# Kernel tuning notes

Hardware: AMD Instinct MI355X
Metric: run time of the kernel (lower is better)

The kernel has to match this reference:

```python
import jax, jax.numpy as jnp
import numpy as np

E = 65536      # num edges
T = 262144     # num triplets
H = 128        # hidden_channels
D = 64         # int_emb_size
C = 8          # basis_emb_size
NR = 6         # num_radial
NS = 7         # num_spherical
NB = 6         # len(bt_list) = num_BT + 1
BT_LIST = (-1, 0, 1, 2, 3, 4)
NBS = 1        # num_before_skip (also used for after-skip list in original code)


def setup_inputs() -> dict:
    key = jax.random.key(0)
    ks = iter(jax.random.split(key, 40))
    s = 0.05
    p = lambda shape: jax.random.normal(next(ks), shape, dtype=jnp.float32) * s
    inp = dict(
        x=jax.random.normal(next(ks), (E, H), dtype=jnp.float32),
        rbf=jax.random.normal(next(ks), (E, NR), dtype=jnp.float32),
        sbf=jax.random.normal(next(ks), (T, NS * NR), dtype=jnp.float32),
        idx_kj=jax.random.randint(next(ks), (T,), 0, E),
        idx_ji=jax.random.randint(next(ks), (T,), 0, E),
        bt=jax.random.randint(next(ks), (E,), 0, 5),
        lambda_d=1,
        alpha=jnp.float32(0.7),
        # per-branch stacked weights (6 branches)
        W_kj=p((NB, H, H)), b_kj=jnp.zeros((NB, H), jnp.float32),
        W_rbf1=p((NB, NR, C)), W_rbf2=p((NB, C, H)),
        W_sbf1=p((NB, NS * NR, C)), W_sbf2=p((NB, C, D)),
        W_down=p((NB, H, D)),
        W_ji=p((H, H)), b_ji=jnp.zeros((H,), jnp.float32),
        W_up=p((D, H)),
        rb1_w=p((NBS, H, H)), rb1_b=jnp.zeros((NBS, H), jnp.float32),
        rb2_w=p((NBS, H, H)), rb2_b=jnp.zeros((NBS, H), jnp.float32),
        W_lin=p((H, H)), b_lin=jnp.zeros((H,), jnp.float32),
        ra1_w=p((NBS, H, H)), ra1_b=jnp.zeros((NBS, H), jnp.float32),
        ra2_w=p((NBS, H, H)), ra2_b=jnp.zeros((NBS, H), jnp.float32),
    )
    return inp


def reference(x, rbf, sbf, idx_kj, idx_ji, bt, lambda_d, alpha,
              W_kj, b_kj, W_rbf1, W_rbf2, W_sbf1, W_sbf2, W_down,
              W_ji, b_ji, W_up, rb1_w, rb1_b, rb2_w, rb2_b,
              W_lin, b_lin, ra1_w, ra1_b, ra2_w, ra2_b):
    act = jax.nn.silu

    x_ji = act(x @ W_ji + b_ji)                                  # [E,H]

    # per-branch edge transforms, vectorized over the 6 branches (axis b)
    tmp = act(jnp.einsum('eh,bhg->beg', x, W_kj) + b_kj[:, None, :])   # [B,E,H]
    rbf_p = jnp.einsum('er,brc->bec', rbf, W_rbf1)                     # [B,E,C]
    rbf_p = jnp.einsum('bec,bcg->beg', rbf_p, W_rbf2)                  # [B,E,H]
    tmp = tmp * rbf_p
    down = act(jnp.einsum('beh,bhd->bed', tmp, W_down))                # [B,E,D]

    sbf_p = jnp.einsum('ts,bsc->btc', sbf, W_sbf1)                     # [B,T,C]
    sbf_p = jnp.einsum('btc,bcd->btd', sbf_p, W_sbf2)                  # [B,T,D]

    spe = down[:, idx_kj, :] * sbf_p                                   # [B,T,D]

    # last branch scattered with weight alpha
    x_kj_tot = alpha * jax.ops.segment_sum(spe[-1], idx_ji, num_segments=E)

    # per band-type masked scatter with weight (1 - alpha)
    bt_trip = bt[idx_kj]                                               # [T]
    for b, btv in enumerate(BT_LIST):
        m = (bt_trip == btv).astype(x.dtype)[:, None]
        x_kj_tot = x_kj_tot + (1.0 - alpha) * jax.ops.segment_sum(
            spe[b] * m, idx_ji, num_segments=E)

    x_kj = act(x_kj_tot @ W_up)                                        # [E,H]
    h = x_ji + x_kj
    for i in range(rb1_w.shape[0]):
        h = h + act(act(h @ rb1_w[i] + rb1_b[i]) @ rb2_w[i] + rb2_b[i])
    h = act(h @ W_lin + b_lin) + x
    for i in range(ra1_w.shape[0]):
        h = h + act(act(h @ ra1_w[i] + ra1_b[i]) @ ra2_w[i] + ra2_b[i])
    return h
```

## Files before the change

kernel.cpp:

```cpp
#include <hip/hip_runtime.h>
#include <hip/hip_bf16.h>
#include <stdint.h>

typedef __bf16 bf16_t;
typedef bf16_t bf16x8 __attribute__((ext_vector_type(8)));
typedef bf16_t bf16x2 __attribute__((ext_vector_type(2)));
typedef float f32x4 __attribute__((ext_vector_type(4)));

#define E_N 65536
#define T_N 262144
#define CAP 16
#define OVF_MAX T_N

__device__ __forceinline__ float silu_f(float v) {
  return v / (1.0f + __expf(-v));
}

__device__ __forceinline__ int permrow(int n) {
  return (n & ~31) | ((n & 1) << 4) | ((n & 30) >> 1);
}

__device__ __forceinline__ uint32_t pack_bf16(float a, float b) {
  union { bf16x2 h; uint32_t u; } u;
  u.h[0] = (bf16_t)a; u.h[1] = (bf16_t)b;
  return u.u;
}

template<int KI, int NTJ>
__device__ __forceinline__ void gemm_tile(const bf16_t* A, const bf16_t* B,
                                          int mb, int nb, int l16, int q,
                                          f32x4 (&acc)[2][NTJ]) {
#pragma unroll
  for (int kt = 0; kt < KI; ++kt) {
    const int sw = ((kt * 4 + q) ^ l16) << 3;
    bf16x8 a0 = *(const bf16x8*)(A + ((mb + l16) << 7) + sw);
    bf16x8 a1 = *(const bf16x8*)(A + ((mb + 16 + l16) << 7) + sw);
#pragma unroll
    for (int tj = 0; tj < NTJ; ++tj) {
      bf16x8 b = *(const bf16x8*)(B + ((nb + tj * 16 + l16) << 7) + sw);
      acc[0][tj] = __builtin_amdgcn_mfma_f32_16x16x32_bf16(a0, b, acc[0][tj], 0, 0, 0);
      acc[1][tj] = __builtin_amdgcn_mfma_f32_16x16x32_bf16(a1, b, acc[1][tj], 0, 0, 0);
    }
  }
}

template<int ROWS, int K8>
__device__ __forceinline__ void load_wT(bf16_t* dst, const bf16_t* src, int tid) {
  const uint4* s = (const uint4*)src;
#pragma unroll
  for (int i = tid; i < ROWS * K8; i += 256) {
    const int n = i / K8, k8 = i % K8;
    const int row = permrow(n);
    *(uint4*)(dst + (row << 7) + ((k8 ^ (row & 15)) << 3)) = s[i];
  }
}

template<int C4>
__device__ __forceinline__ void stage_x(bf16_t* dst, const float* src, int tid) {
  const float4* g = (const float4*)src;
#pragma unroll
  for (int i = tid; i < 64 * C4; i += 256) {
    const int row = i / C4, c4 = i % C4;
    float4 v = g[i];
    bf16_t t[4] = {(bf16_t)v.x, (bf16_t)v.y, (bf16_t)v.z, (bf16_t)v.w};
    *(uint2*)(dst + (row << 7) + ((((c4 >> 1) ^ (row & 15)) << 3) | ((c4 & 1) << 2))) =
        *(const uint2*)t;
  }
}

__global__ void prep_kernel(
    const float* __restrict__ W_ji, const float* __restrict__ W_kj,
    const float* __restrict__ W_down, const float* __restrict__ W_up,
    const float* __restrict__ rb1, const float* __restrict__ rb2,
    const float* __restrict__ W_lin, const float* __restrict__ ra1,
    const float* __restrict__ ra2, const float* __restrict__ W_rbf1,
    const float* __restrict__ W_rbf2,
    bf16_t* __restrict__ wjiT, bf16_t* __restrict__ wkjT,
    bf16_t* __restrict__ wdownT, bf16_t* __restrict__ wupT,
    bf16_t* __restrict__ rb1T, bf16_t* __restrict__ rb2T,
    bf16_t* __restrict__ linT, bf16_t* __restrict__ ra1T,
    bf16_t* __restrict__ ra2T, bf16_t* __restrict__ wcb)
{
  const int tid = threadIdx.x;
  if (blockIdx.x >= 112) {
    const int o = (blockIdx.x - 112) * 256 + tid;
    if (o < 640) {
      const int b = o >> 7, n = o & 127;
      bf16_t t[8];
#pragma unroll
      for (int r = 0; r < 6; ++r) {
        const float* w1 = W_rbf1 + (b + 1) * 48 + r * 8;
        const float* w2 = W_rbf2 + (b + 1) * 1024 + n;
        float s = 0.f;
#pragma unroll
        for (int c = 0; c < 8; ++c) s += w1[c] * w2[c * 128];
        t[r] = (bf16_t)s;
      }
      t[6] = (bf16_t)0.f; t[7] = (bf16_t)0.f;
      *(uint4*)(wcb + (b * 128 + n) * 8) = *(const uint4*)t;
    }
    return;
  }
  const int c = blockIdx.x * 256 + tid;
  const float* src; bf16_t* dst; int n, k8, N, K;
  if (c < 22528) {
    const int m = c >> 11, w = c & 2047;
    n = w >> 4; k8 = w & 15; N = 128; K = 128;
    if (m == 0)      { src = W_ji;  dst = wjiT; }
    else if (m <= 5) { src = W_kj + m * 16384; dst = wkjT + (m - 1) * 16384; }
    else if (m == 6) { src = rb1;   dst = rb1T; }
    else if (m == 7) { src = rb2;   dst = rb2T; }
    else if (m == 8) { src = W_lin; dst = linT; }
    else if (m == 9) { src = ra1;   dst = ra1T; }
    else             { src = ra2;   dst = ra2T; }
  } else if (c < 27648) {
    const int m = (c - 22528) >> 10, w = (c - 22528) & 1023;
    n = w >> 4; k8 = w & 15; N = 64; K = 128;
    src = W_down + (m + 1) * 8192; dst = wdownT + m * 8192;
  } else {
    const int w = c - 27648;
    n = w >> 3; k8 = w & 7; N = 128; K = 64;
    src = W_up; dst = wupT;
  }
  bf16_t t[8];
#pragma unroll
  for (int j = 0; j < 8; ++j) t[j] = (bf16_t)src[(k8 * 8 + j) * N + n];
  *(uint4*)(dst + n * K + k8 * 8) = *(const uint4*)t;
}

__global__ __launch_bounds__(256, 2)
void edge_kernel(const float* __restrict__ x, const float* __restrict__ rbf,
                 const float* __restrict__ b_kj, const float* __restrict__ b_ji,
                 const bf16_t* __restrict__ wjiT, const bf16_t* __restrict__ wkjT,
                 const bf16_t* __restrict__ wdownT, const bf16_t* __restrict__ wcb,
                 bf16_t* __restrict__ x_ji_out, bf16_t* __restrict__ down)
{
  __shared__ bf16_t xA[64 * 128];
  __shared__ bf16_t Wb[128 * 128];
  __shared__ bf16_t tmpA[64 * 128];
  __shared__ float biasS[128];
  bf16_t* const rbfA = tmpA;
  bf16_t* const WcB  = tmpA + 64 * 40;

  const int tid = threadIdx.x;
  const int lane = tid & 63, wv = tid >> 6;
  const int q = lane >> 4, l16 = lane & 15;
  const int mb = (wv >> 1) * 32, nb = (wv & 1) * 64;
  const int R = blockIdx.x * 64;
  const int br = blockIdx.y;

  stage_x<32>(xA, x + (size_t)R * 128, tid);
  if (br == 0) {
    load_wT<128, 16>(Wb, wjiT, tid);
    if (tid < 128) biasS[tid] = b_ji[tid];
  } else {
    load_wT<128, 16>(Wb, wkjT + (br - 1) * 16384, tid);
    if (tid < 128) biasS[tid] = b_kj[br * 128 + tid];
    const uint4 z = {0, 0, 0, 0};
    if (tid < 64) {
      const float* rg = rbf + (size_t)(R + tid) * 6;
      bf16_t t[8] = {(bf16_t)rg[0], (bf16_t)rg[1], (bf16_t)rg[2],
                     (bf16_t)rg[3], (bf16_t)rg[4], (bf16_t)rg[5],
                     (bf16_t)0.f, (bf16_t)0.f};
      *(uint4*)(rbfA + tid * 40)      = *(const uint4*)t;
      *(uint4*)(rbfA + tid * 40 + 8)  = z;
      *(uint4*)(rbfA + tid * 40 + 16) = z;
      *(uint4*)(rbfA + tid * 40 + 24) = z;
    } else if (tid >= 128) {
      const int n = tid - 128;
      const int row = permrow(n);
      uint4 w = ((const uint4*)(wcb + (size_t)(br - 1) * 1024))[n];
      *(uint4*)(WcB + row * 40)      = w;
      *(uint4*)(WcB + row * 40 + 8)  = z;
      *(uint4*)(WcB + row * 40 + 16) = z;
      *(uint4*)(WcB + row * 40 + 24) = z;
    }
  }
  __syncthreads();

  f32x4 acc[2][4] = {};
  gemm_tile<4, 4>(xA, Wb, mb, nb, l16, q, acc);

  if (br == 0) {
#pragma unroll
    for (int ti = 0; ti < 2; ++ti)
#pragma unroll
      for (int r = 0; r < 4; ++r) {
        const int row = mb + ti * 16 + q * 4 + r;
#pragma unroll
        for (int gl = 0; gl < 2; ++gl) {
          const int col0 = nb + gl * 32 + 2 * l16;
          const float2 b2 = *(const float2*)&biasS[col0];
          *(uint32_t*)&x_ji_out[(size_t)(R + row) * 128 + col0] =
              pack_bf16(silu_f(acc[ti][2 * gl][r] + b2.x),
                        silu_f(acc[ti][2 * gl + 1][r] + b2.y));
        }
      }
    return;
  }

  f32x4 accr[2][4] = {};
  {
    bf16x8 a0 = *(const bf16x8*)(rbfA + (mb + l16) * 40 + q * 8);
    bf16x8 a1 = *(const bf16x8*)(rbfA + (mb + 16 + l16) * 40 + q * 8);
#pragma unroll
    for (int tj = 0; tj < 4; ++tj) {
      bf16x8 b = *(const bf16x8*)(WcB + (nb + tj * 16 + l16) * 40 + q * 8);
      accr[0][tj] = __builtin_amdgcn_mfma_f32_16x16x32_bf16(a0, b, accr[0][tj], 0, 0, 0);
      accr[1][tj] = __builtin_amdgcn_mfma_f32_16x16x32_bf16(a1, b, accr[1][tj], 0, 0, 0);
    }
  }
  __syncthreads();

#pragma unroll
  for (int ti = 0; ti < 2; ++ti)
#pragma unroll
    for (int r = 0; r < 4; ++r) {
      const int row = mb + ti * 16 + q * 4 + r;
#pragma unroll
      for (int gl = 0; gl < 2; ++gl) {
        const int col0 = nb + gl * 32 + 2 * l16;
        const float2 b2 = *(const float2*)&biasS[col0];
        const float v0 = silu_f(acc[ti][2 * gl][r] + b2.x) * accr[ti][2 * gl][r];
        const float v1 = silu_f(acc[ti][2 * gl + 1][r] + b2.y) * accr[ti][2 * gl + 1][r];
        *(uint32_t*)&tmpA[(row << 7) + ((((col0 >> 3) ^ (row & 15)) << 3) | (col0 & 7))] =
            pack_bf16(v0, v1);
      }
    }
  __syncthreads();
  load_wT<64, 16>(xA, wdownT + (br - 1) * 8192, tid);
  __syncthreads();

  const int nb2 = (wv & 1) * 32;
  f32x4 acc2[2][2] = {};
  gemm_tile<4, 2>(tmpA, xA, mb, nb2, l16, q, acc2);
#pragma unroll
  for (int ti = 0; ti < 2; ++ti)
#pragma unroll
    for (int r = 0; r < 4; ++r) {
      const int row = mb + ti * 16 + q * 4 + r;
      const int col0 = nb2 + 2 * l16;
      *(uint32_t*)&down[((size_t)(br - 1) * E_N + R + row) * 64 + col0] =
          pack_bf16(silu_f(acc2[ti][0][r]), silu_f(acc2[ti][1][r]));
    }
}

__global__ __launch_bounds__(256, 4)
void c8_kernel(const float* __restrict__ sbf, const int* __restrict__ idx_kj,
               const int* __restrict__ idx_ji, const int* __restrict__ bt,
               const float* __restrict__ Wsbf1,
               float* __restrict__ c8g, uint32_t* __restrict__ meta,
               int* __restrict__ cnt, int* __restrict__ list,
               int* __restrict__ ovf)
{
  __shared__ float s_sbf[64 * 44];
  __shared__ float s_W1[2016];
  __shared__ float s_c8[64 * 16];
  __shared__ int s_bs[64];

  const int tid = threadIdx.x;
  const int base = blockIdx.x * 64;

  for (int i = tid; i < 2016; i += 256) s_W1[i] = Wsbf1[i];
  if (tid < 64) {
    const int t = base + tid;
    const int kj = idx_kj[t];
    const int ji = idx_ji[t];
    const int bs = bt[kj] + 1;
    s_bs[tid] = bs;
    meta[t] = (uint32_t)kj | ((uint32_t)bs << 16);
    const int pos = atomicAdd(&cnt[ji], 1);
    if (pos < CAP) {
      list[ji * CAP + pos] = t;
    } else {
      const int o = atomicAdd(&ovf[0], 1);
      if (o < OVF_MAX) { ovf[2 + 2 * o] = t; ovf[2 + 2 * o + 1] = ji; }
    }
  }
  {
    const float2* sg = (const float2*)(sbf + (size_t)base * 42);
    for (int i = tid; i < 64 * 21; i += 256) {
      const int r = i / 21, c2 = i - r * 21;
      const float2 v = sg[i];
      s_sbf[r * 44 + c2 * 2] = v.x;
      s_sbf[r * 44 + c2 * 2 + 1] = v.y;
    }
  }
  __syncthreads();

  {
    const int i = tid >> 2;
    const int brr = (tid >> 1) & 1;
    const int cg = tid & 1;
    const int b = brr ? s_bs[i] : 5;
    const float* w = &s_W1[b * 336 + cg * 4];
    const float* sb = &s_sbf[i * 44];
    float a0 = 0.f, a1 = 0.f, a2 = 0.f, a3 = 0.f;
#pragma unroll
    for (int s = 0; s < 42; ++s) {
      const float sv = sb[s];
      const float* ws = w + s * 8;
      a0 += sv * ws[0]; a1 += sv * ws[1]; a2 += sv * ws[2]; a3 += sv * ws[3];
    }
    float* dc = &s_c8[i * 16 + brr * 8 + cg * 4];
    dc[0] = a0; dc[1] = a1; dc[2] = a2; dc[3] = a3;
  }
  __syncthreads();

  {
    const float4* s4 = (const float4*)s_c8;
    float4* g4 = (float4*)(c8g + (size_t)base * 16);
    g4[tid] = s4[tid];
  }
}

__global__ __launch_bounds__(256, 8)
void gather_kernel(const int* __restrict__ cnt, const int* __restrict__ list,
                   const uint32_t* __restrict__ meta, const float* __restrict__ c8g,
                   const float* __restrict__ Wsbf2, const bf16_t* __restrict__ down,
                   const float* __restrict__ alpha_p, const int* __restrict__ ovf,
                   float* __restrict__ xkj)
{
  __shared__ float sW2[3072];
  for (int i = threadIdx.x; i < 3072; i += 256) sW2[i] = Wsbf2[i];
  __syncthreads();

  const int e = blockIdx.x * 4 + (threadIdx.x >> 6);
  const int j = threadIdx.x & 63;
  const float alpha = alpha_p[0], oma = 1.f - alpha;
  const float* w5 = &sW2[5 * 512 + j];

  float acc = 0.f;
  int n = cnt[e];
  if (n > CAP) n = CAP;
#pragma unroll 2
  for (int k = 0; k < n; ++k) {
    const int t = __builtin_amdgcn_readfirstlane(list[e * CAP + k]);
    const uint32_t m = __builtin_amdgcn_readfirstlane(meta[t]);
    const int kj = m & 0xffff;
    const int b  = m >> 16;
    const float g5 = (float)down[((size_t)4 * E_N + kj) * 64 + j];
    const float gb = (float)down[((size_t)(b - 1) * E_N + kj) * 64 + j];
    const float* cp = c8g + (size_t)t * 16;
    float d5 = 0.f, db = 0.f;
#pragma unroll
    for (int c = 0; c < 8; ++c) {
      d5 += cp[c]     * w5[c * 64];
      db += cp[8 + c] * sW2[b * 512 + c * 64 + j];
    }
    acc += alpha * g5 * d5 + oma * gb * db;
  }

  const int oc = ovf[0];
  for (int k = 0; k < oc; ++k) {
    const int ji = ovf[2 + 2 * k + 1];
    if (ji != e) continue;
    const int t = ovf[2 + 2 * k];
    const uint32_t m = meta[t];
    const int kj = m & 0xffff;
    const int b  = m >> 16;
    const float g5 = (float)down[((size_t)4 * E_N + kj) * 64 + j];
    const float gb = (float)down[((size_t)(b - 1) * E_N + kj) * 64 + j];
    const float* cp = c8g + (size_t)t * 16;
    float d5 = 0.f, db = 0.f;
#pragma unroll
    for (int c = 0; c < 8; ++c) {
      d5 += cp[c]     * w5[c * 64];
      db += cp[8 + c] * sW2[b * 512 + c * 64 + j];
    }
    acc += alpha * g5 * d5 + oma * gb * db;
  }

  xkj[(size_t)e * 64 + j] = acc;
}

__global__ __launch_bounds__(256, 2)
void epi_kernel(const float* __restrict__ x, const bf16_t* __restrict__ x_ji,
                const float* __restrict__ xkj,
                const bf16_t* __restrict__ wupT,
                const bf16_t* __restrict__ rb1T, const float* __restrict__ rb1_b,
                const bf16_t* __restrict__ rb2T, const float* __restrict__ rb2_b,
                const bf16_t* __restrict__ linT, const float* __restrict__ lin_b,
                const bf16_t* __restrict__ ra1T, const float* __restrict__ ra1_b,
                const bf16_t* __restrict__ ra2T, const float* __restrict__ ra2_b,
                float* __restrict__ out)
{
  __shared__ bf16_t bufA[64 * 128];
  __shared__ bf16_t bufB[64 * 128];
  __shared__ bf16_t Wb[128 * 128];
  __shared__ float biasS[128];

  const int tid = threadIdx.x;
  const int lane = tid & 63, wv = tid >> 6;
  const int q = lane >> 4, l16 = lane & 15;
  const int mb = (wv >> 1) * 32, nb = (wv & 1) * 64;
  const int R = blockIdx.x * 64;

  stage_x<16>(bufA, xkj + (size_t)R * 64, tid);
  load_wT<128, 8>(Wb, wupT, tid);
  __syncthreads();

  f32x4 hreg[2][4];
  {
    f32x4 acc[2][4] = {};
    gemm_tile<2, 4>(bufA, Wb, mb, nb, l16, q, acc);
#pragma unroll
    for (int ti = 0; ti < 2; ++ti)
#pragma unroll
      for (int r = 0; r < 4; ++r) {
        const int row = mb + ti * 16 + q * 4 + r;
#pragma unroll
        for (int gl = 0; gl < 2; ++gl) {
          const int col0 = nb + gl * 32 + 2 * l16;
          union { uint32_t u; bf16x2 h; } xj;
          xj.u = *(const uint32_t*)&x_ji[(size_t)(R + row) * 128 + col0];
          const float h0 = (float)xj.h[0] + silu_f(acc[ti][2 * gl][r]);
          const float h1 = (float)xj.h[1] + silu_f(acc[ti][2 * gl + 1][r]);
          hreg[ti][2 * gl][r] = h0;
          hreg[ti][2 * gl + 1][r] = h1;
          *(uint32_t*)&bufB[(row << 7) + ((((col0 >> 3) ^ (row & 15)) << 3) | (col0 & 7))] =
              pack_bf16(h0, h1);
        }
      }
  }

#define EPI_STAGE(ASRC, WSRC, BIAS, BODY)                                        \
  __syncthreads();                                                               \
  load_wT<128, 16>(Wb, WSRC, tid);                                               \
  if (tid < 128) biasS[tid] = BIAS[tid];                                         \
  __syncthreads();                                                               \
  {                                                                              \
    f32x4 acc[2][4] = {};                                                        \
    gemm_tile<4, 4>(ASRC, Wb, mb, nb, l16, q, acc);                              \
    _Pragma("unroll")                                                            \
    for (int ti = 0; ti < 2; ++ti)                                               \
      _Pragma("unroll")                                                          \
      for (int r = 0; r < 4; ++r) {                                              \
        const int row = mb + ti * 16 + q * 4 + r;                                \
        _Pragma("unroll")                                                        \
        for (int gl = 0; gl < 2; ++gl) {                                         \
          const int col0 = nb + gl * 32 + 2 * l16;                               \
          const float2 b2 = *(const float2*)&biasS[col0];                        \
          const float g0 = acc[ti][2 * gl][r] + b2.x;                            \
          const float g1 = acc[ti][2 * gl + 1][r] + b2.y;                        \
          BODY                                                                   \
        }                                                                        \
      }                                                                          \
  }

  EPI_STAGE(bufB, rb1T, rb1_b, {
    *(uint32_t*)&bufA[(row << 7) + ((((col0 >> 3) ^ (row & 15)) << 3) | (col0 & 7))] =
        pack_bf16(silu_f(g0), silu_f(g1));
  })

  EPI_STAGE(bufA, rb2T, rb2_b, {
    const float h0 = hreg[ti][2 * gl][r] + silu_f(g0);
    const float h1 = hreg[ti][2 * gl + 1][r] + silu_f(g1);
    hreg[ti][2 * gl][r] = h0; hreg[ti][2 * gl + 1][r] = h1;
    *(uint32_t*)&bufB[(row << 7) + ((((col0 >> 3) ^ (row & 15)) << 3) | (col0 & 7))] =
        pack_bf16(h0, h1);
  })

  EPI_STAGE(bufB, linT, lin_b, {
    const float2 xv = *(const float2*)&x[(size_t)(R + row) * 128 + col0];
    const float h0 = silu_f(g0) + xv.x;
    const float h1 = silu_f(g1) + xv.y;
    hreg[ti][2 * gl][r] = h0; hreg[ti][2 * gl + 1][r] = h1;
    *(uint32_t*)&bufA[(row << 7) + ((((col0 >> 3) ^ (row & 15)) << 3) | (col0 & 7))] =
        pack_bf16(h0, h1);
  })

  EPI_STAGE(bufA, ra1T, ra1_b, {
    *(uint32_t*)&bufB[(row << 7) + ((((col0 >> 3) ^ (row & 15)) << 3) | (col0 & 7))] =
        pack_bf16(silu_f(g0), silu_f(g1));
  })

  EPI_STAGE(bufB, ra2T, ra2_b, {
    float2 o;
    o.x = hreg[ti][2 * gl][r] + silu_f(g0);
    o.y = hreg[ti][2 * gl + 1][r] + silu_f(g1);
    *(float2*)&out[(size_t)(R + row) * 128 + col0] = o;
  })
#undef EPI_STAGE
}

extern "C" void kernel_launch(void* const* d_in, const int* in_sizes, int n_in,
                              void* d_out, int out_size, void* d_ws, size_t ws_size,
                              hipStream_t stream)
{
  (void)in_sizes; (void)n_in; (void)out_size; (void)ws_size;
  const float* x      = (const float*)d_in[0];
  const float* rbf    = (const float*)d_in[1];
  const float* sbf    = (const float*)d_in[2];
  const int*   idx_kj = (const int*)d_in[3];
  const int*   idx_ji = (const int*)d_in[4];
  const int*   bt     = (const int*)d_in[5];
  const float* alpha  = (const float*)d_in[7];
  const float* W_kj   = (const float*)d_in[8];
  const float* b_kj   = (const float*)d_in[9];
  const float* W_rbf1 = (const float*)d_in[10];
  const float* W_rbf2 = (const float*)d_in[11];
  const float* W_sbf1 = (const float*)d_in[12];
  const float* W_sbf2 = (const float*)d_in[13];
  const float* W_down = (const float*)d_in[14];
  const float* W_ji   = (const float*)d_in[15];
  const float* b_ji   = (const float*)d_in[16];
  const float* W_up   = (const float*)d_in[17];
  const float* rb1_w  = (const float*)d_in[18];
  const float* rb1_b  = (const float*)d_in[19];
  const float* rb2_w  = (const float*)d_in[20];
  const float* rb2_b  = (const float*)d_in[21];
  const float* W_lin  = (const float*)d_in[22];
  const float* b_lin  = (const float*)d_in[23];
  const float* ra1_w  = (const float*)d_in[24];
  const float* ra1_b  = (const float*)d_in[25];
  const float* ra2_w  = (const float*)d_in[26];
  const float* ra2_b  = (const float*)d_in[27];

  char* ws = (char*)d_ws;
  bf16_t* down   = (bf16_t*)(ws);
  bf16_t* x_ji   = (bf16_t*)(ws + 41943040);
  float*  xkj    = (float*) (ws + 58720256);
  char* wbase    = ws + 75497472;
  bf16_t* wjiT   = (bf16_t*)(wbase + 0);
  bf16_t* wkjT   = (bf16_t*)(wbase + 32768);
  bf16_t* wdownT = (bf16_t*)(wbase + 196608);
  bf16_t* wupT   = (bf16_t*)(wbase + 278528);
  bf16_t* rb1T   = (bf16_t*)(wbase + 294912);
  bf16_t* rb2T   = (bf16_t*)(wbase + 327680);
  bf16_t* linT   = (bf16_t*)(wbase + 360448);
  bf16_t* ra1T   = (bf16_t*)(wbase + 393216);
  bf16_t* ra2T   = (bf16_t*)(wbase + 425984);
  bf16_t* wcb    = (bf16_t*)(wbase + 458752);
  float*    c8g  = (float*)   (ws + 75966464);
  uint32_t* meta = (uint32_t*)(ws + 92743680);
  int*      list = (int*)     (ws + 93792256);
  int*      cnt  = (int*)     (ws + 97986560);
  int*      ovf  = (int*)     (ws + 98248704);

  hipMemsetAsync(cnt, 0, 262144 + 8, stream);
  prep_kernel<<<115, 256, 0, stream>>>(W_ji, W_kj, W_down, W_up, rb1_w, rb2_w,
                                       W_lin, ra1_w, ra2_w, W_rbf1, W_rbf2,
                                       wjiT, wkjT, wdownT, wupT, rb1T, rb2T,
                                       linT, ra1T, ra2T, wcb);
  edge_kernel<<<dim3(E_N / 64, 6), 256, 0, stream>>>(x, rbf, b_kj, b_ji, wjiT,
                                                     wkjT, wdownT, wcb, x_ji, down);
  c8_kernel<<<T_N / 64, 256, 0, stream>>>(sbf, idx_kj, idx_ji, bt, W_sbf1,
                                          c8g, meta, cnt, list, ovf);
  gather_kernel<<<E_N / 4 / 64, 256, 0, stream>>>(cnt, list, meta, c8g, W_sbf2,
                                                  down, alpha, ovf, xkj);
  epi_kernel<<<E_N / 64, 256, 0, stream>>>(x, x_ji, xkj, wupT, rb1T, rb1_b,
                                           rb2T, rb2_b, linT, b_lin,
                                           ra1T, ra1_b, ra2T, ra2_b,
                                           (float*)d_out);
}
```

Baseline: 340.9 us.

## Pre-swizzle weight images and double-buffer them into LDS via async global_load_lds

The prep kernel now writes each weight set, with bias, Wdown and combined rbf weights, already permuted and swizzled into contiguous LDS-ready images. The edge kernel loops over all six branches in one block instead of one block per branch, so the x tile is staged once per row block. Weight images are streamed with global_load_lds into two LDS slots, so the next branch's weights load while the current one computes. The epilogue kernel uses the same double-buffered scheme for its five 128x128 stages. In exchange, LDS use per block roughly doubles and launch bounds drop to one block per CU, which cuts occupancy and latency hiding, and parallelism across branches becomes serial work within a block.

New measurement: 362.9 us. 6.4% more time.

```diff
diff --git a/kernel.cpp b/kernel.cpp
--- a/kernel.cpp
+++ b/kernel.cpp
@@ -12,6 +12,9 @@
 #define CAP 16
 #define OVF_MAX T_N
 
+#define ESET_BYTES 61440
+#define PSET_BYTES 36864
+
 __device__ __forceinline__ float silu_f(float v) {
   return v / (1.0f + __expf(-v));
 }
@@ -26,6 +29,23 @@
   return u.u;
 }
 
+__device__ __forceinline__ void g2l16(const void* g, void* l) {
+  __builtin_amdgcn_global_load_lds(
+      (const __attribute__((address_space(1))) void*)g,
+      (__attribute__((address_space(3))) void*)l, 16, 0, 0);
+}
+
+template<int CHUNKS>
+__device__ __forceinline__ void dma_copy(const char* g, char* l, int wv, int lane) {
+#pragma unroll
+  for (int c = 0; c < CHUNKS / 4; ++c) {
+    const int off = (c * 4 + wv) * 1024 + lane * 16;
+    g2l16(g + off, l + off);
+  }
+}
+
+#define VMCNT0()  asm volatile("s_waitcnt vmcnt(0)" ::: "memory")
+
 template<int KI, int NTJ>
 __device__ __forceinline__ void gemm_tile(const bf16_t* A, const bf16_t* B,
                                           int mb, int nb, int l16, int q,
@@ -41,17 +61,6 @@
       acc[0][tj] = __builtin_amdgcn_mfma_f32_16x16x32_bf16(a0, b, acc[0][tj], 0, 0, 0);
       acc[1][tj] = __builtin_amdgcn_mfma_f32_16x16x32_bf16(a1, b, acc[1][tj], 0, 0, 0);
     }
-  }
-}
-
-template<int ROWS, int K8>
-__device__ __forceinline__ void load_wT(bf16_t* dst, const bf16_t* src, int tid) {
-  const uint4* s = (const uint4*)src;
-#pragma unroll
-  for (int i = tid; i < ROWS * K8; i += 256) {
-    const int n = i / K8, k8 = i % K8;
-    const int row = permrow(n);
-    *(uint4*)(dst + (row << 7) + ((k8 ^ (row & 15)) << 3)) = s[i];
   }
 }
 
@@ -75,15 +84,53 @@
     const float* __restrict__ W_lin, const float* __restrict__ ra1,
     const float* __restrict__ ra2, const float* __restrict__ W_rbf1,
     const float* __restrict__ W_rbf2,
-    bf16_t* __restrict__ wjiT, bf16_t* __restrict__ wkjT,
-    bf16_t* __restrict__ wdownT, bf16_t* __restrict__ wupT,
-    bf16_t* __restrict__ rb1T, bf16_t* __restrict__ rb2T,
-    bf16_t* __restrict__ linT, bf16_t* __restrict__ ra1T,
-    bf16_t* __restrict__ ra2T, bf16_t* __restrict__ wcb)
+    const float* __restrict__ b_ji, const float* __restrict__ b_kj,
+    const float* __restrict__ rb1_b, const float* __restrict__ rb2_b,
+    const float* __restrict__ b_lin, const float* __restrict__ ra1_b,
+    const float* __restrict__ ra2_b,
+    char* __restrict__ esets, char* __restrict__ psets)
 {
   const int tid = threadIdx.x;
-  if (blockIdx.x >= 112) {
-    const int o = (blockIdx.x - 112) * 256 + tid;
+  const int blk = blockIdx.x;
+
+  if (blk < 88) {
+    const int item = blk * 256 + tid;
+    const int m = item >> 11, w = item & 2047;
+    const int n = w >> 4, k8 = w & 15;
+    const float* src; char* img;
+    if (m == 0)      { src = W_ji;             img = esets; }
+    else if (m <= 5) { src = W_kj + m * 16384; img = esets + m * ESET_BYTES; }
+    else if (m == 6) { src = rb1;   img = psets + 1 * PSET_BYTES; }
+    else if (m == 7) { src = rb2;   img = psets + 2 * PSET_BYTES; }
+    else if (m == 8) { src = W_lin; img = psets + 3 * PSET_BYTES; }
+    else if (m == 9) { src = ra1;   img = psets + 4 * PSET_BYTES; }
+    else             { src = ra2;   img = psets + 5 * PSET_BYTES; }
+    bf16_t t[8];
+#pragma unroll
+    for (int j = 0; j < 8; ++j) t[j] = (bf16_t)src[(k8 * 8 + j) * 128 + n];
+    const int row = permrow(n);
+    *(uint4*)((bf16_t*)img + (row << 7) + ((k8 ^ (row & 15)) << 3)) = *(const uint4*)t;
+  } else if (blk < 108) {
+    const int item = (blk - 88) * 256 + tid;
+    const int m = item >> 10, w = item & 1023;
+    const int n = w >> 4, k8 = w & 15;
+    const float* src = W_down + (m + 1) * 8192;
+    bf16_t* img = (bf16_t*)(esets + (m + 1) * ESET_BYTES + 32768);
+    bf16_t t[8];
+#pragma unroll
+    for (int j = 0; j < 8; ++j) t[j] = (bf16_t)src[(k8 * 8 + j) * 64 + n];
+    const int row = permrow(n);
+    *(uint4*)(img + (row << 7) + ((k8 ^ (row & 15)) << 3)) = *(const uint4*)t;
+  } else if (blk < 112) {
+    const int item = (blk - 108) * 256 + tid;
+    const int n = item >> 3, k8 = item & 7;
+    bf16_t t[8];
+#pragma unroll
+    for (int j = 0; j < 8; ++j) t[j] = (bf16_t)W_up[(k8 * 8 + j) * 128 + n];
+    const int row = permrow(n);
+    *(uint4*)((bf16_t*)psets + (row << 7) + ((k8 ^ (row & 15)) << 3)) = *(const uint4*)t;
+  } else if (blk < 115) {
+    const int o = (blk - 112) * 256 + tid;
     if (o < 640) {
       const int b = o >> 7, n = o & 127;
       bf16_t t[8];
@@ -97,152 +144,137 @@
         t[r] = (bf16_t)s;
       }
       t[6] = (bf16_t)0.f; t[7] = (bf16_t)0.f;
-      *(uint4*)(wcb + (b * 128 + n) * 8) = *(const uint4*)t;
-    }
-    return;
-  }
-  const int c = blockIdx.x * 256 + tid;
-  const float* src; bf16_t* dst; int n, k8, N, K;
-  if (c < 22528) {
-    const int m = c >> 11, w = c & 2047;
-    n = w >> 4; k8 = w & 15; N = 128; K = 128;
-    if (m == 0)      { src = W_ji;  dst = wjiT; }
-    else if (m <= 5) { src = W_kj + m * 16384; dst = wkjT + (m - 1) * 16384; }
-    else if (m == 6) { src = rb1;   dst = rb1T; }
-    else if (m == 7) { src = rb2;   dst = rb2T; }
-    else if (m == 8) { src = W_lin; dst = linT; }
-    else if (m == 9) { src = ra1;   dst = ra1T; }
-    else             { src = ra2;   dst = ra2T; }
-  } else if (c < 27648) {
-    const int m = (c - 22528) >> 10, w = (c - 22528) & 1023;
-    n = w >> 4; k8 = w & 15; N = 64; K = 128;
-    src = W_down + (m + 1) * 8192; dst = wdownT + m * 8192;
+      bf16_t* img = (bf16_t*)(esets + (b + 1) * ESET_BYTES + 49152);
+      const int row = permrow(n);
+      const uint4 z = {0, 0, 0, 0};
+      *(uint4*)(img + row * 40)      = *(const uint4*)t;
+      *(uint4*)(img + row * 40 + 8)  = z;
+      *(uint4*)(img + row * 40 + 16) = z;
+      *(uint4*)(img + row * 40 + 24) = z;
+    }
   } else {
-    const int w = c - 27648;
-    n = w >> 3; k8 = w & 7; N = 128; K = 64;
-    src = W_up; dst = wupT;
-  }
-  bf16_t t[8];
-#pragma unroll
-  for (int j = 0; j < 8; ++j) t[j] = (bf16_t)src[(k8 * 8 + j) * N + n];
-  *(uint4*)(dst + n * K + k8 * 8) = *(const uint4*)t;
-}
-
-__global__ __launch_bounds__(256, 2)
+    const int n = tid & 127;
+    for (int v = (tid >> 7); v < 11; v += 2) {
+      float val; char* dst;
+      if (v == 0)      { val = b_ji[n];          dst = esets + 59392; }
+      else if (v <= 5) { val = b_kj[v * 128 + n]; dst = esets + v * ESET_BYTES + 59392; }
+      else {
+        const float* bs = (v == 6) ? rb1_b : (v == 7) ? rb2_b :
+                          (v == 8) ? b_lin : (v == 9) ? ra1_b : ra2_b;
+        val = bs[n]; dst = psets + (v - 5) * PSET_BYTES + 32768;
+      }
+      ((float*)dst)[n] = val;
+    }
+  }
+}
+
+__global__ __launch_bounds__(256, 1)
 void edge_kernel(const float* __restrict__ x, const float* __restrict__ rbf,
-                 const float* __restrict__ b_kj, const float* __restrict__ b_ji,
-                 const bf16_t* __restrict__ wjiT, const bf16_t* __restrict__ wkjT,
-                 const bf16_t* __restrict__ wdownT, const bf16_t* __restrict__ wcb,
+                 const char* __restrict__ esets,
                  bf16_t* __restrict__ x_ji_out, bf16_t* __restrict__ down)
 {
-  __shared__ bf16_t xA[64 * 128];
-  __shared__ bf16_t Wb[128 * 128];
-  __shared__ bf16_t tmpA[64 * 128];
-  __shared__ float biasS[128];
-  bf16_t* const rbfA = tmpA;
-  bf16_t* const WcB  = tmpA + 64 * 40;
+  __shared__ __align__(16) bf16_t xA[64 * 128];
+  __shared__ __align__(16) bf16_t tmpA[64 * 128];
+  __shared__ __align__(16) bf16_t rbfA[64 * 40];
+  __shared__ __align__(16) char Wset[2][ESET_BYTES];
 
   const int tid = threadIdx.x;
   const int lane = tid & 63, wv = tid >> 6;
   const int q = lane >> 4, l16 = lane & 15;
   const int mb = (wv >> 1) * 32, nb = (wv & 1) * 64;
   const int R = blockIdx.x * 64;
-  const int br = blockIdx.y;
 
   stage_x<32>(xA, x + (size_t)R * 128, tid);
-  if (br == 0) {
-    load_wT<128, 16>(Wb, wjiT, tid);
-    if (tid < 128) biasS[tid] = b_ji[tid];
-  } else {
-    load_wT<128, 16>(Wb, wkjT + (br - 1) * 16384, tid);
-    if (tid < 128) biasS[tid] = b_kj[br * 128 + tid];
+  if (tid < 64) {
+    const float* rg = rbf + (size_t)(R + tid) * 6;
+    bf16_t t[8] = {(bf16_t)rg[0], (bf16_t)rg[1], (bf16_t)rg[2],
+                   (bf16_t)rg[3], (bf16_t)rg[4], (bf16_t)rg[5],
+                   (bf16_t)0.f, (bf16_t)0.f};
     const uint4 z = {0, 0, 0, 0};
-    if (tid < 64) {
-      const float* rg = rbf + (size_t)(R + tid) * 6;
-      bf16_t t[8] = {(bf16_t)rg[0], (bf16_t)rg[1], (bf16_t)rg[2],
-                     (bf16_t)rg[3], (bf16_t)rg[4], (bf16_t)rg[5],
-                     (bf16_t)0.f, (bf16_t)0.f};
-      *(uint4*)(rbfA + tid * 40)      = *(const uint4*)t;
-      *(uint4*)(rbfA + tid * 40 + 8)  = z;
-      *(uint4*)(rbfA + tid * 40 + 16) = z;
-      *(uint4*)(rbfA + tid * 40 + 24) = z;
-    } else if (tid >= 128) {
-      const int n = tid - 128;
-      const int row = permrow(n);
-      uint4 w = ((const uint4*)(wcb + (size_t)(br - 1) * 1024))[n];
-      *(uint4*)(WcB + row * 40)      = w;
-      *(uint4*)(WcB + row * 40 + 8)  = z;
-      *(uint4*)(WcB + row * 40 + 16) = z;
-      *(uint4*)(WcB + row * 40 + 24) = z;
-    }
-  }
+    *(uint4*)(rbfA + tid * 40)      = *(const uint4*)t;
+    *(uint4*)(rbfA + tid * 40 + 8)  = z;
+    *(uint4*)(rbfA + tid * 40 + 16) = z;
+    *(uint4*)(rbfA + tid * 40 + 24) = z;
+  }
+  VMCNT0();
+  dma_copy<60>(esets,              (char*)Wset[0], wv, lane);
+  dma_copy<60>(esets + ESET_BYTES, (char*)Wset[1], wv, lane);
+  asm volatile("s_waitcnt vmcnt(15)" ::: "memory");
   __syncthreads();
 
-  f32x4 acc[2][4] = {};
-  gemm_tile<4, 4>(xA, Wb, mb, nb, l16, q, acc);
-
-  if (br == 0) {
-#pragma unroll
-    for (int ti = 0; ti < 2; ++ti)
-#pragma unroll
-      for (int r = 0; r < 4; ++r) {
-        const int row = mb + ti * 16 + q * 4 + r;
-#pragma unroll
-        for (int gl = 0; gl < 2; ++gl) {
-          const int col0 = nb + gl * 32 + 2 * l16;
-          const float2 b2 = *(const float2*)&biasS[col0];
-          *(uint32_t*)&x_ji_out[(size_t)(R + row) * 128 + col0] =
-              pack_bf16(silu_f(acc[ti][2 * gl][r] + b2.x),
-                        silu_f(acc[ti][2 * gl + 1][r] + b2.y));
+  for (int br = 0; br < 6; ++br) {
+    const char* slot = Wset[br & 1];
+    const bf16_t* Wm  = (const bf16_t*)slot;
+    const bf16_t* Wdn = (const bf16_t*)(slot + 32768);
+    const bf16_t* Wcb = (const bf16_t*)(slot + 49152);
+    const float* biasS = (const float*)(slot + 59392);
+
+    f32x4 acc[2][4] = {};
+    gemm_tile<4, 4>(xA, Wm, mb, nb, l16, q, acc);
+
+    if (br == 0) {
+#pragma unroll
+      for (int ti = 0; ti < 2; ++ti)
+#pragma unroll
+        for (int r = 0; r < 4; ++r) {
+          const int row = mb + ti * 16 + q * 4 + r;
+#pragma unroll
+          for (int gl = 0; gl < 2; ++gl) {
+            const int col0 = nb + gl * 32 + 2 * l16;
+            const float2 b2 = *(const float2*)&biasS[col0];
+            *(uint32_t*)&x_ji_out[(size_t)(R + row) * 128 + col0] =
+                pack_bf16(silu_f(acc[ti][2 * gl][r] + b2.x),
+                          silu_f(acc[ti][2 * gl + 1][r] + b2.y));
+          }
+        }
+    } else {
+      f32x4 accr[2][4] = {};
+      {
+        bf16x8 a0 = *(const bf16x8*)(rbfA + (mb + l16) * 40 + q * 8);
+        bf16x8 a1 = *(const bf16x8*)(rbfA + (mb + 16 + l16) * 40 + q * 8);
+#pragma unroll
+        for (int tj = 0; tj < 4; ++tj) {
+          bf16x8 b = *(const bf16x8*)(Wcb + (nb + tj * 16 + l16) * 40 + q * 8);
+          accr[0][tj] = __builtin_amdgcn_mfma_f32_16x16x32_bf16(a0, b, accr[0][tj], 0, 0, 0);
+          accr[1][tj] = __builtin_amdgcn_mfma_f32_16x16x32_bf16(a1, b, accr[1][tj], 0, 0, 0);
         }
       }
-    return;
-  }
-
-  f32x4 accr[2][4] = {};
-  {
-    bf16x8 a0 = *(const bf16x8*)(rbfA + (mb + l16) * 40 + q * 8);
-    bf16x8 a1 = *(const bf16x8*)(rbfA + (mb + 16 + l16) * 40 + q * 8);
-#pragma unroll
-    for (int tj = 0; tj < 4; ++tj) {
-      bf16x8 b = *(const bf16x8*)(WcB + (nb + tj * 16 + l16) * 40 + q * 8);
-      accr[0][tj] = __builtin_amdgcn_mfma_f32_16x16x32_bf16(a0, b, accr[0][tj], 0, 0, 0);
-      accr[1][tj] = __builtin_amdgcn_mfma_f32_16x16x32_bf16(a1, b, accr[1][tj], 0, 0, 0);
-    }
-  }
-  __syncthreads();
-
-#pragma unroll
-  for (int ti = 0; ti < 2; ++ti)
-#pragma unroll
-    for (int r = 0; r < 4; ++r) {
-      const int row = mb + ti * 16 + q * 4 + r;
-#pragma unroll
-      for (int gl = 0; gl < 2; ++gl) {
-        const int col0 = nb + gl * 32 + 2 * l16;
-        const float2 b2 = *(const float2*)&biasS[col0];
-        const float v0 = silu_f(acc[ti][2 * gl][r] + b2.x) * accr[ti][2 * gl][r];
-        const float v1 = silu_f(acc[ti][2 * gl + 1][r] + b2.y) * accr[ti][2 * gl + 1][r];
-        *(uint32_t*)&tmpA[(row << 7) + ((((col0 >> 3) ^ (row & 15)) << 3) | (col0 & 7))] =
-            pack_bf16(v0, v1);
-      }
-    }
-  __syncthreads();
-  load_wT<64, 16>(xA, wdownT + (br - 1) * 8192, tid);
-  __syncthreads();
-
-  const int nb2 = (wv & 1) * 32;
-  f32x4 acc2[2][2] = {};
-  gemm_tile<4, 2>(tmpA, xA, mb, nb2, l16, q, acc2);
-#pragma unroll
-  for (int ti = 0; ti < 2; ++ti)
-#pragma unroll
-    for (int r = 0; r < 4; ++r) {
-      const int row = mb + ti * 16 + q * 4 + r;
-      const int col0 = nb2 + 2 * l16;
-      *(uint32_t*)&down[((size_t)(br - 1) * E_N + R + row) * 64 + col0] =
-          pack_bf16(silu_f(acc2[ti][0][r]), silu_f(acc2[ti][1][r]));
-    }
+#pragma unroll
+      for (int ti = 0; ti < 2; ++ti)
+#pragma unroll
+        for (int r = 0; r < 4; ++r) {
+          const int row = mb + ti * 16 + q * 4 + r;
+#pragma unroll
+          for (int gl = 0; gl < 2; ++gl) {
+            const int col0 = nb + gl * 32 + 2 * l16;
+            const float2 b2 = *(const float2*)&biasS[col0];
+            const float v0 = silu_f(acc[ti][2 * gl][r] + b2.x) * accr[ti][2 * gl][r];
+            const float v1 = silu_f(acc[ti][2 * gl + 1][r] + b2.y) * accr[ti][2 * gl + 1][r];
+            *(uint32_t*)&tmpA[(row << 7) + ((((col0 >> 3) ^ (row & 15)) << 3) | (col0 & 7))] =
+                pack_bf16(v0, v1);
+          }
+        }
+      __syncthreads();
+
+      const int nb2 = (wv & 1) * 32;
+      f32x4 acc2[2][2] = {};
+      gemm_tile<4, 2>(tmpA, Wdn, mb, nb2, l16, q, acc2);
+#pragma unroll
+      for (int ti = 0; ti < 2; ++ti)
+#pragma unroll
+        for (int r = 0; r < 4; ++r) {
+          const int row = mb + ti * 16 + q * 4 + r;
+          const int col0 = nb2 + 2 * l16;
+          *(uint32_t*)&down[((size_t)(br - 1) * E_N + R + row) * 64 + col0] =
+              pack_bf16(silu_f(acc2[ti][0][r]), silu_f(acc2[ti][1][r]));
+        }
+    }
+
+    VMCNT0();
+    __syncthreads();
+    if (br < 4)
+      dma_copy<60>(esets + (size_t)(br + 2) * ESET_BYTES, (char*)Wset[br & 1], wv, lane);
+  }
 }
 
 __global__ __launch_bounds__(256, 4)
@@ -374,21 +406,14 @@
   xkj[(size_t)e * 64 + j] = acc;
 }
 
-__global__ __launch_bounds__(256, 2)
+__global__ __launch_bounds__(256, 1)
 void epi_kernel(const float* __restrict__ x, const bf16_t* __restrict__ x_ji,
-                const float* __restrict__ xkj,
-                const bf16_t* __restrict__ wupT,
-                const bf16_t* __restrict__ rb1T, const float* __restrict__ rb1_b,
-                const bf16_t* __restrict__ rb2T, const float* __restrict__ rb2_b,
-                const bf16_t* __restrict__ linT, const float* __restrict__ lin_b,
-                const bf16_t* __restrict__ ra1T, const float* __restrict__ ra1_b,
-                const bf16_t* __restrict__ ra2T, const float* __restrict__ ra2_b,
+                const float* __restrict__ xkj, const char* __restrict__ psets,
                 float* __restrict__ out)
 {
-  __shared__ bf16_t bufA[64 * 128];
-  __shared__ bf16_t bufB[64 * 128];
-  __shared__ bf16_t Wb[128 * 128];
-  __shared__ float biasS[128];
+  __shared__ __align__(16) bf16_t bufA[64 * 128];
+  __shared__ __align__(16) bf16_t bufB[64 * 128];
+  __shared__ __align__(16) char Wset[2][PSET_BYTES];
 
   const int tid = threadIdx.x;
   const int lane = tid & 63, wv = tid >> 6;
@@ -397,13 +422,16 @@
   const int R = blockIdx.x * 64;
 
   stage_x<16>(bufA, xkj + (size_t)R * 64, tid);
-  load_wT<128, 8>(Wb, wupT, tid);
+  VMCNT0();
+  dma_copy<36>(psets,              (char*)Wset[0], wv, lane);
+  dma_copy<36>(psets + PSET_BYTES, (char*)Wset[1], wv, lane);
+  asm volatile("s_waitcnt vmcnt(9)" ::: "memory");
   __syncthreads();
 
   f32x4 hreg[2][4];
   {
     f32x4 acc[2][4] = {};
-    gemm_tile<2, 4>(bufA, Wb, mb, nb, l16, q, acc);
+    gemm_tile<2, 4>(bufA, (const bf16_t*)Wset[0], mb, nb, l16, q, acc);
 #pragma unroll
     for (int ti = 0; ti < 2; ++ti)
 #pragma unroll
@@ -423,15 +451,16 @@
         }
       }
   }
-
-#define EPI_STAGE(ASRC, WSRC, BIAS, BODY)                                        \
-  __syncthreads();                                                               \
-  load_wT<128, 16>(Wb, WSRC, tid);                                               \
-  if (tid < 128) biasS[tid] = BIAS[tid];                                         \
-  __syncthreads();                                                               \
+  VMCNT0();
+  __syncthreads();
+  dma_copy<36>(psets + 2 * PSET_BYTES, (char*)Wset[0], wv, lane);
+
+#define EPI_STAGE(K, ASRC, BODY)                                                 \
   {                                                                              \
+    const char* slot_ = Wset[(K) & 1];                                           \
+    const float* biasS = (const float*)(slot_ + 32768);                          \
     f32x4 acc[2][4] = {};                                                        \
-    gemm_tile<4, 4>(ASRC, Wb, mb, nb, l16, q, acc);                              \
+    gemm_tile<4, 4>(ASRC, (const bf16_t*)slot_, mb, nb, l16, q, acc);            \
     _Pragma("unroll")                                                            \
     for (int ti = 0; ti < 2; ++ti)                                               \
       _Pragma("unroll")                                                          \
@@ -446,14 +475,18 @@
           BODY                                                                   \
         }                                                                        \
       }                                                                          \
-  }
-
-  EPI_STAGE(bufB, rb1T, rb1_b, {
+  }                                                                              \
+  VMCNT0();                                                                      \
+  __syncthreads();                                                               \
+  if ((K) + 2 <= 5)                                                              \
+    dma_copy<36>(psets + ((K) + 2) * PSET_BYTES, (char*)Wset[(K) & 1], wv, lane);
+
+  EPI_STAGE(1, bufB, {
     *(uint32_t*)&bufA[(row << 7) + ((((col0 >> 3) ^ (row & 15)) << 3) | (col0 & 7))] =
         pack_bf16(silu_f(g0), silu_f(g1));
   })
 
-  EPI_STAGE(bufA, rb2T, rb2_b, {
+  EPI_STAGE(2, bufA, {
     const float h0 = hreg[ti][2 * gl][r] + silu_f(g0);
     const float h1 = hreg[ti][2 * gl + 1][r] + silu_f(g1);
     hreg[ti][2 * gl][r] = h0; hreg[ti][2 * gl + 1][r] = h1;
@@ -461,7 +494,7 @@
         pack_bf16(h0, h1);
   })
 
-  EPI_STAGE(bufB, linT, lin_b, {
+  EPI_STAGE(3, bufB, {
     const float2 xv = *(const float2*)&x[(size_t)(R + row) * 128 + col0];
     const float h0 = silu_f(g0) + xv.x;
     const float h1 = silu_f(g1) + xv.y;
@@ -470,12 +503,12 @@
         pack_bf16(h0, h1);
   })
 
-  EPI_STAGE(bufA, ra1T, ra1_b, {
+  EPI_STAGE(4, bufA, {
     *(uint32_t*)&bufB[(row << 7) + ((((col0 >> 3) ^ (row & 15)) << 3) | (col0 & 7))] =
         pack_bf16(silu_f(g0), silu_f(g1));
   })
 
-  EPI_STAGE(bufB, ra2T, ra2_b, {
+  EPI_STAGE(5, bufB, {
     float2 o;
     o.x = hreg[ti][2 * gl][r] + silu_f(g0);
     o.y = hreg[ti][2 * gl + 1][r] + silu_f(g1);
@@ -521,36 +554,23 @@
   bf16_t* down   = (bf16_t*)(ws);
   bf16_t* x_ji   = (bf16_t*)(ws + 41943040);
   float*  xkj    = (float*) (ws + 58720256);
-  char* wbase    = ws + 75497472;
-  bf16_t* wjiT   = (bf16_t*)(wbase + 0);
-  bf16_t* wkjT   = (bf16_t*)(wbase + 32768);
-  bf16_t* wdownT = (bf16_t*)(wbase + 196608);
-  bf16_t* wupT   = (bf16_t*)(wbase + 278528);
-  bf16_t* rb1T   = (bf16_t*)(wbase + 294912);
-  bf16_t* rb2T   = (bf16_t*)(wbase + 327680);
-  bf16_t* linT   = (bf16_t*)(wbase + 360448);
-  bf16_t* ra1T   = (bf16_t*)(wbase + 393216);
-  bf16_t* ra2T   = (bf16_t*)(wbase + 425984);
-  bf16_t* wcb    = (bf16_t*)(wbase + 458752);
-  float*    c8g  = (float*)   (ws + 75966464);
-  uint32_t* meta = (uint32_t*)(ws + 92743680);
-  int*      list = (int*)     (ws + 93792256);
-  int*      cnt  = (int*)     (ws + 97986560);
-  int*      ovf  = (int*)     (ws + 98248704);
+  char*   esets  = ws + 75497472;
+  char*   psets  = ws + 75866112;
+  float*    c8g  = (float*)   (ws + 76087296);
+  uint32_t* meta = (uint32_t*)(ws + 92864512);
+  int*      list = (int*)     (ws + 93913088);
+  int*      cnt  = (int*)     (ws + 98107392);
+  int*      ovf  = (int*)     (ws + 98369536);
 
   hipMemsetAsync(cnt, 0, 262144 + 8, stream);
-  prep_kernel<<<115, 256, 0, stream>>>(W_ji, W_kj, W_down, W_up, rb1_w, rb2_w,
+  prep_kernel<<<116, 256, 0, stream>>>(W_ji, W_kj, W_down, W_up, rb1_w, rb2_w,
                                        W_lin, ra1_w, ra2_w, W_rbf1, W_rbf2,
-                                       wjiT, wkjT, wdownT, wupT, rb1T, rb2T,
-                                       linT, ra1T, ra2T, wcb);
-  edge_kernel<<<dim3(E_N / 64, 6), 256, 0, stream>>>(x, rbf, b_kj, b_ji, wjiT,
-                                                     wkjT, wdownT, wcb, x_ji, down);
+                                       b_ji, b_kj, rb1_b, rb2_b, b_lin,
+                                       ra1_b, ra2_b, esets, psets);
+  edge_kernel<<<E_N / 64, 256, 0, stream>>>(x, rbf, esets, x_ji, down);
   c8_kernel<<<T_N / 64, 256, 0, stream>>>(sbf, idx_kj, idx_ji, bt, W_sbf1,
                                           c8g, meta, cnt, list, ovf);
   gather_kernel<<<E_N / 4 / 64, 256, 0, stream>>>(cnt, list, meta, c8g, W_sbf2,
                                                   down, alpha, ovf, xkj);
-  epi_kernel<<<E_N / 64, 256, 0, stream>>>(x, x_ji, xkj, wupT, rb1T, rb1_b,
-                                           rb2T, rb2_b, linT, b_lin,
-                                           ra1T, ra1_b, ra2T, ra2_b,
-                                           (float*)d_out);
-}
+  epi_kernel<<<E_N / 64, 256, 0, stream>>>(x, x_ji, xkj, psets, (float*)d_out);
+}
```
